# Kernel optimization log

Hardware: AMD Instinct MI355X
Metric: run time of the kernel (lower is better)

Reference implementation:

```python
import jax, jax.numpy as jnp
import numpy as np
import math

B, N, D, SEQ = 4, 1024, 512, 256
HID, DIST_D, N_NER, N_LAB = 150, 128, 3, 4
SPANS_PER_WORD = 0.5
ASPECT, OPINION = 1, 2
NUM_DIST_EMB = 512


def setup_inputs() -> dict:
    key = jax.random.key(0)
    ks = jax.random.split(key, 9)
    starts = jax.random.randint(ks[0], (B, N), 0, SEQ)
    widths = jax.random.randint(ks[1], (B, N), 0, 8)
    ends = jnp.clip(starts + widths, 0, SEQ - 1)
    spans = jnp.stack([starts, ends], axis=-1).astype(jnp.int32)  # [B,N,2]
    ner_scores = jax.random.normal(ks[2], (B, N, N_NER), jnp.float32)
    span_embeddings = jax.random.normal(ks[3], (B, N, D), jnp.float32)
    span_mask = jnp.ones((B, N), dtype=bool)

    pair_dim = 2 * D + DIST_D

    def xavier(k, shape):
        std = math.sqrt(2.0 / (shape[0] + shape[1]))
        return jax.random.normal(k, shape, jnp.float32) * std

    dist_table = xavier(ks[4], (NUM_DIST_EMB, DIST_D))
    W1 = xavier(ks[5], (pair_dim, HID)); b1 = jnp.zeros((HID,), jnp.float32)
    W2 = xavier(ks[6], (HID, HID));      b2 = jnp.zeros((HID,), jnp.float32)
    Wc = xavier(ks[7], (HID, N_LAB));    bc = jnp.zeros((N_LAB,), jnp.float32)

    return dict(spans=spans, ner_scores=ner_scores, span_embeddings=span_embeddings,
                span_mask=span_mask, seq_length=SEQ, dist_table=dist_table,
                W1=W1, b1=b1, W2=W2, b2=b2, Wc=Wc, bc=bc)


def bucket_values(d, num_identity=4, num_total=10):
    # semi-logscale buckets: [0,1,2,3,4,5-7,8-15,16-31,32-63,64+]
    logspace = jnp.floor(jnp.log2(jnp.maximum(d, 1).astype(jnp.float32))).astype(jnp.int32) + (num_identity - 1)
    return jnp.clip(jnp.where(d <= num_identity, d, logspace), 0, num_total - 1)


def _prune(scores, mask, k):
    masked = jnp.where(mask, scores, jnp.float32(-1e20))
    _, idx = jax.lax.top_k(masked, k)  # [B,k]
    return idx


def reference(spans, ner_scores, span_embeddings, span_mask, seq_length,
              dist_table, W1, b1, W2, b2, Wc, bc):
    bsz, n_spans, d = span_embeddings.shape
    k = min(int(math.ceil(seq_length * SPANS_PER_WORD)), n_spans)

    a_idx = _prune(ner_scores[..., ASPECT], span_mask, k)    # [B,k]
    o_idx = _prune(ner_scores[..., OPINION], span_mask, k)
    a_keep = jnp.ones((bsz, k), dtype=bool)  # uniform seq_length -> all kept
    o_keep = a_keep

    gather = lambda t, i: jnp.take_along_axis(t, i[..., None], axis=1)
    a_emb = gather(span_embeddings, a_idx)   # [B,k,D]
    o_emb = gather(span_embeddings, o_idx)   # [B,k,D]
    spans_a = gather(spans, a_idx)           # [B,k,2]
    spans_o = gather(spans, o_idx)           # [B,k,2]

    # pairwise min span distance -> bucket -> embedding
    dis1 = jnp.abs(spans_a[..., 0][:, :, None] - spans_o[..., 1][:, None, :])
    dis2 = jnp.abs(spans_a[..., 1][:, :, None] - spans_o[..., 0][:, None, :])
    dis = jnp.minimum(dis1, dis2)                      # [B,k,k]
    dist_emb = dist_table[bucket_values(dis)]          # [B,k,k,DIST_D]

    pair = jnp.concatenate([
        jnp.broadcast_to(a_emb[:, :, None, :], (bsz, k, k, d)),
        jnp.broadcast_to(o_emb[:, None, :, :], (bsz, k, k, d)),
        dist_emb,
    ], axis=-1)                                        # [B,k,k,2D+DIST_D]

    # FeedForward (2 layers, ReLU, dropout=identity at eval) + classifier
    h = jax.nn.relu(pair @ W1 + b1)
    h = jax.nn.relu(h @ W2 + b2)
    scores = h @ Wc + bc                               # [B,k,k,n_labels]

    rel_mask = a_keep[:, :, None] & o_keep[:, None, :]
    return (jax.nn.softmax(scores, axis=-1), rel_mask, pair, spans_a, spans_o)
```

## Files before the change

### kernel.cpp

```cpp
#include <hip/hip_runtime.h>
#include <hip/hip_bf16.h>

#define BB 4
#define NN 1024
#define DD 512
#define KK 128
#define HID 150
#define HIDP 160
#define HSTRIDE 168
#define DIST_D 128
#define PAIRD 1152

typedef __attribute__((ext_vector_type(4))) float f32x4;
typedef __attribute__((ext_vector_type(8))) short s16x8;

__global__ __launch_bounds__(1024) void k_topk(const int* __restrict__ spans,
                                               const float* __restrict__ ner,
                                               const float* __restrict__ dist_table,
                                               const float* __restrict__ W1,
                                               const float* __restrict__ b1,
                                               const float* __restrict__ W2,
                                               int* ws_aidx, int* ws_oidx,
                                               int* ws_sa, int* ws_so,
                                               float* ws_cd, __hip_bfloat16* ws_w2t,
                                               float* out3, float* out4) {
    int t = threadIdx.x;
    int bx = blockIdx.x;
    if (bx < 8) {
        __shared__ unsigned long long sk[NN];
        int b = bx >> 1;
        int which = bx & 1;
        int ch = which ? 2 : 1;
        float v = ner[(b * NN + t) * 3 + ch];
        unsigned int u = __float_as_uint(v);
        unsigned int s = (u & 0x80000000u) ? ~u : (u ^ 0x80000000u);
        sk[t] = ((unsigned long long)s << 32) | (unsigned int)(NN - 1 - t);
        for (int ksz = 2; ksz <= NN; ksz <<= 1) {
            for (int jsz = ksz >> 1; jsz > 0; jsz >>= 1) {
                __syncthreads();
                int ixj = t ^ jsz;
                if (ixj > t) {
                    unsigned long long k1 = sk[t], k2 = sk[ixj];
                    bool before = k1 > k2;
                    bool desc = ((t & ksz) == 0);
                    if (desc ? !before : before) { sk[t] = k2; sk[ixj] = k1; }
                }
            }
        }
        __syncthreads();
        if (t < KK) {
            int idx = NN - 1 - (int)(unsigned int)(sk[t] & 0xffffffffu);
            int s0 = spans[(b * NN + idx) * 2];
            int s1 = spans[(b * NN + idx) * 2 + 1];
            int row = b * KK + t;
            if (which == 0) {
                ws_aidx[row] = idx;
                ws_sa[row * 2] = s0; ws_sa[row * 2 + 1] = s1;
                out3[row * 2] = (float)s0; out3[row * 2 + 1] = (float)s1;
            } else {
                ws_oidx[row] = idx;
                ws_so[row * 2] = s0; ws_so[row * 2 + 1] = s1;
                out4[row * 2] = (float)s0; out4[row * 2 + 1] = (float)s1;
            }
        }
    } else if (bx < 18) {
        int bk = bx - 8;
        if (t < HIDP) {
            float acc = 0.f;
            if (t < HID) {
                acc = b1[t];
                for (int d = 0; d < DIST_D; ++d)
                    acc = fmaf(dist_table[bk * DIST_D + d], W1[(size_t)(2 * DD + d) * HID + t], acc);
            }
            ws_cd[bk * HIDP + t] = acc;
        }
    } else {
        int e = (bx - 18) * 1024 + t;
        if (e < HIDP * HSTRIDE) {
            int n = e / HSTRIDE, d = e - n * HSTRIDE;
            float v = (n < HID && d < HID) ? W2[d * HID + n] : 0.f;
            ws_w2t[e] = __float2bfloat16(v);
        }
    }
}

__global__ __launch_bounds__(256) void k_contrib(const float* __restrict__ emb,
                                                 const float* __restrict__ W1,
                                                 const int* __restrict__ ws_aidx,
                                                 const int* __restrict__ ws_oidx,
                                                 float* ws_ca, float* ws_co) {
    __shared__ __align__(16) float es[4][DD];
    int t = threadIdx.x;
    int bx = blockIdx.x;
    int which = bx >> 7;
    int row0 = (bx & 127) * 4;
    const int* idxsrc = which ? ws_oidx : ws_aidx;
    for (int x = t; x < 512; x += 256) {
        int r = x >> 7, c = x & 127;
        int row = row0 + r;
        int b = row >> 7;
        int idx = idxsrc[row];
        ((float4*)es[r])[c] = ((const float4*)(emb + ((size_t)(b * NN) + idx) * DD))[c];
    }
    __syncthreads();
    if (t < HIDP) {
        float a0 = 0.f, a1 = 0.f, a2 = 0.f, a3 = 0.f;
        if (t < HID) {
            const float* w = W1 + (size_t)(which * DD) * HID + t;
#pragma unroll 4
            for (int d4 = 0; d4 < 128; ++d4) {
                float4 e0 = ((const float4*)es[0])[d4];
                float4 e1 = ((const float4*)es[1])[d4];
                float4 e2 = ((const float4*)es[2])[d4];
                float4 e3 = ((const float4*)es[3])[d4];
                float w0 = w[(size_t)(4 * d4 + 0) * HID];
                float w1v = w[(size_t)(4 * d4 + 1) * HID];
                float w2v = w[(size_t)(4 * d4 + 2) * HID];
                float w3 = w[(size_t)(4 * d4 + 3) * HID];
                a0 = fmaf(e0.x, w0, a0); a0 = fmaf(e0.y, w1v, a0); a0 = fmaf(e0.z, w2v, a0); a0 = fmaf(e0.w, w3, a0);
                a1 = fmaf(e1.x, w0, a1); a1 = fmaf(e1.y, w1v, a1); a1 = fmaf(e1.z, w2v, a1); a1 = fmaf(e1.w, w3, a1);
                a2 = fmaf(e2.x, w0, a2); a2 = fmaf(e2.y, w1v, a2); a2 = fmaf(e2.z, w2v, a2); a2 = fmaf(e2.w, w3, a2);
                a3 = fmaf(e3.x, w0, a3); a3 = fmaf(e3.y, w1v, a3); a3 = fmaf(e3.z, w2v, a3); a3 = fmaf(e3.w, w3, a3);
            }
        }
        float* dstb = which ? ws_co : ws_ca;
        dstb[(row0 + 0) * HIDP + t] = a0;
        dstb[(row0 + 1) * HIDP + t] = a1;
        dstb[(row0 + 2) * HIDP + t] = a2;
        dstb[(row0 + 3) * HIDP + t] = a3;
    }
}

__global__ __launch_bounds__(256) void k_pair(const float* __restrict__ emb,
                                              const float* __restrict__ dist_table,
                                              const int* __restrict__ ws_aidx,
                                              const int* __restrict__ ws_oidx,
                                              const int* __restrict__ ws_sa,
                                              const int* __restrict__ ws_so,
                                              float* __restrict__ out1,
                                              float* __restrict__ out2) {
    int t = threadIdx.x;
    int blk = blockIdx.x;
    int bi = blk >> 3, jc = blk & 7;
    int b = bi >> 7;
    int j0 = jc << 4;
    int c = t & 127;
    int half = t >> 7;

    const float4* ebase = (const float4*)(emb + (size_t)b * NN * DD);

    int aidx = ws_aidx[bi];
    float4 areg = ebase[(size_t)aidx * 128 + c];

    float4 oreg[8];
#pragma unroll
    for (int it = 0; it < 8; ++it) {
        int j = it * 2 + half;
        int oidx = ws_oidx[b * KK + j0 + j];
        oreg[it] = ebase[(size_t)oidx * 128 + c];
    }

    int sa0 = ws_sa[bi * 2], sa1 = ws_sa[bi * 2 + 1];
    float4 dreg[2];
    int dj[2], dc[2];
#pragma unroll
    for (int it = 0; it < 2; ++it) {
        int x = it * 256 + t;
        dj[it] = x >> 5; dc[it] = x & 31;
        int so0 = ws_so[(b * KK + j0 + dj[it]) * 2];
        int so1 = ws_so[(b * KK + j0 + dj[it]) * 2 + 1];
        int dd = min(abs(sa0 - so1), abs(sa1 - so0));
        int bkt = (dd <= 4) ? dd : min(34 - __clz(dd), 9);
        dreg[it] = ((const float4*)dist_table)[bkt * 32 + dc[it]];
    }

    if (t < 16) out1[bi * KK + j0 + t] = 1.0f;

    float4* dst = (float4*)(out2 + (size_t)bi * (KK * PAIRD)) + (size_t)j0 * 288;
#pragma unroll
    for (int it = 0; it < 8; ++it) {
        int j = it * 2 + half;
        dst[j * 288 + c] = areg;
        dst[j * 288 + 128 + c] = oreg[it];
    }
#pragma unroll
    for (int it = 0; it < 2; ++it) {
        dst[dj[it] * 288 + 256 + dc[it]] = dreg[it];
    }
}

__global__ __launch_bounds__(256) void k_score(const float* __restrict__ Wc,
                                               const float* __restrict__ bcp,
                                               const float* __restrict__ b2p,
                                               const int* __restrict__ ws_sa,
                                               const int* __restrict__ ws_so,
                                               const float* __restrict__ ws_ca,
                                               const float* __restrict__ ws_co,
                                               const float* __restrict__ ws_cd,
                                               const __hip_bfloat16* __restrict__ ws_w2t,
                                               float* __restrict__ out0) {
    __shared__ float ca_s[HIDP];
    __shared__ float wc_s[HID * 4];
    __shared__ float b2_s[HIDP];
    __shared__ float bc_s[4];
    __shared__ int bkt_s[KK];
    __shared__ __align__(16) __hip_bfloat16 h1_s[KK * HSTRIDE];

    int t = threadIdx.x;
    int bi = blockIdx.x;
    int b = bi >> 7;

    if (t < HIDP) ca_s[t] = ws_ca[bi * HIDP + t];
    int sa0 = ws_sa[bi * 2], sa1 = ws_sa[bi * 2 + 1];
    if (t < KK) {
        int so0 = ws_so[(b * KK + t) * 2], so1 = ws_so[(b * KK + t) * 2 + 1];
        int dd = min(abs(sa0 - so1), abs(sa1 - so0));
        bkt_s[t] = (dd <= 4) ? dd : min(34 - __clz(dd), 9);
    }
    for (int x = t; x < HID * 4; x += 256) wc_s[x] = Wc[x];
    if (t < HIDP) b2_s[t] = (t < HID) ? b2p[t] : 0.f;
    if (t < 4) bc_s[t] = bcp[t];
    __syncthreads();

    for (int x = t; x < KK * HIDP; x += 256) {
        int j = x / HIDP, n = x - j * HIDP;
        float v = ca_s[n] + ws_co[(size_t)(b * KK + j) * HIDP + n] + ws_cd[bkt_s[j] * HIDP + n];
        h1_s[j * HSTRIDE + n] = __float2bfloat16(fmaxf(v, 0.f));
    }
    __syncthreads();

    int wave = t >> 6, l = t & 63;
    int lc = l & 15, lg = l >> 4;
    f32x4 acc[2][10];
#pragma unroll
    for (int mi = 0; mi < 2; ++mi)
#pragma unroll
        for (int nt = 0; nt < 10; ++nt)
            acc[mi][nt] = (f32x4){0.f, 0.f, 0.f, 0.f};

#pragma unroll
    for (int kk = 0; kk < 5; ++kk) {
        s16x8 af0 = *(const s16x8*)&h1_s[(wave * 32 + lc) * HSTRIDE + kk * 32 + lg * 8];
        s16x8 af1 = *(const s16x8*)&h1_s[(wave * 32 + 16 + lc) * HSTRIDE + kk * 32 + lg * 8];
#pragma unroll
        for (int nt = 0; nt < 10; ++nt) {
            s16x8 bf = *(const s16x8*)&ws_w2t[(nt * 16 + lc) * HSTRIDE + kk * 32 + lg * 8];
            acc[0][nt] = __builtin_amdgcn_mfma_f32_16x16x32_bf16(af0, bf, acc[0][nt], 0, 0, 0);
            acc[1][nt] = __builtin_amdgcn_mfma_f32_16x16x32_bf16(af1, bf, acc[1][nt], 0, 0, 0);
        }
    }

#pragma unroll
    for (int mi = 0; mi < 2; ++mi) {
#pragma unroll
        for (int r = 0; r < 4; ++r) {
            int j = wave * 32 + mi * 16 + lg * 4 + r;
            float p0 = 0.f, p1 = 0.f, p2 = 0.f, p3 = 0.f;
#pragma unroll
            for (int nt = 0; nt < 10; ++nt) {
                int n = nt * 16 + lc;
                if (n < HID) {
                    float h2 = fmaxf(acc[mi][nt][r] + b2_s[n], 0.f);
                    p0 = fmaf(h2, wc_s[n * 4 + 0], p0);
                    p1 = fmaf(h2, wc_s[n * 4 + 1], p1);
                    p2 = fmaf(h2, wc_s[n * 4 + 2], p2);
                    p3 = fmaf(h2, wc_s[n * 4 + 3], p3);
                }
            }
#pragma unroll
            for (int m = 8; m >= 1; m >>= 1) {
                p0 += __shfl_xor(p0, m, 16);
                p1 += __shfl_xor(p1, m, 16);
                p2 += __shfl_xor(p2, m, 16);
                p3 += __shfl_xor(p3, m, 16);
            }
            p0 += bc_s[0]; p1 += bc_s[1]; p2 += bc_s[2]; p3 += bc_s[3];
            float mx = fmaxf(fmaxf(p0, p1), fmaxf(p2, p3));
            float e0 = expf(p0 - mx), e1 = expf(p1 - mx), e2 = expf(p2 - mx), e3 = expf(p3 - mx);
            float inv = 1.f / (e0 + e1 + e2 + e3);
            if (lc < 4) {
                float v = (lc == 0) ? e0 : (lc == 1) ? e1 : (lc == 2) ? e2 : e3;
                out0[((size_t)bi * KK + j) * 4 + lc] = v * inv;
            }
        }
    }
}

extern "C" void kernel_launch(void* const* d_in, const int* in_sizes, int n_in,
                              void* d_out, int out_size, void* d_ws, size_t ws_size,
                              hipStream_t stream) {
    const int*   spans = (const int*)d_in[0];
    const float* ner   = (const float*)d_in[1];
    const float* emb   = (const float*)d_in[2];
    const float* dist_table = (const float*)d_in[5];
    const float* W1 = (const float*)d_in[6];
    const float* b1 = (const float*)d_in[7];
    const float* W2 = (const float*)d_in[8];
    const float* b2 = (const float*)d_in[9];
    const float* Wc = (const float*)d_in[10];
    const float* bc = (const float*)d_in[11];

    float* out0 = (float*)d_out;
    float* out1 = out0 + (size_t)BB * KK * KK * 4;
    float* out2 = out1 + (size_t)BB * KK * KK;
    float* out3 = out2 + (size_t)BB * KK * KK * PAIRD;
    float* out4 = out3 + (size_t)BB * KK * 2;

    int* ws_aidx = (int*)d_ws;
    int* ws_oidx = ws_aidx + BB * KK;
    int* ws_sa   = ws_oidx + BB * KK;
    int* ws_so   = ws_sa + BB * KK * 2;
    float* ws_ca = (float*)(ws_so + BB * KK * 2);
    float* ws_co = ws_ca + BB * KK * HIDP;
    float* ws_cd = ws_co + BB * KK * HIDP;
    __hip_bfloat16* ws_w2t = (__hip_bfloat16*)(ws_cd + 16 * HIDP);

    k_topk<<<45, 1024, 0, stream>>>(spans, ner, dist_table, W1, b1, W2,
                                    ws_aidx, ws_oidx, ws_sa, ws_so,
                                    ws_cd, ws_w2t, out3, out4);
    k_contrib<<<256, 256, 0, stream>>>(emb, W1, ws_aidx, ws_oidx, ws_ca, ws_co);
    k_pair<<<BB * KK * 8, 256, 0, stream>>>(emb, dist_table, ws_aidx, ws_oidx, ws_sa, ws_so,
                                            out1, out2);
    k_score<<<BB * KK, 256, 0, stream>>>(Wc, bc, b2, ws_sa, ws_so,
                                         ws_ca, ws_co, ws_cd, ws_w2t, out0);
}
```

Measured before the change: 113.4 us.

## Fuse pair-write and score kernels; replace bitonic top-k with rank counting

Merges the pair-tensor writer and the MLP scoring kernel into one launch that interleaves one score block per eight copy blocks, so the compute-bound scoring can overlap the bandwidth-bound pair writes. The first-layer activations are now built directly in MFMA fragment registers from global memory instead of being staged through shared memory, and the weight-transpose row stride changes. Top-k switches from a full bitonic sort with many barriers to each thread counting how many keys exceed its own, giving its rank in a single pass. The cost is more global reads per score wave and O(N) shared-memory reads per thread in top-k.

Result: faster. 104.2 us (-8.1%).

```diff
diff --git a/kernel.cpp b/kernel.cpp
--- a/kernel.cpp
+++ b/kernel.cpp
@@ -7,12 +7,16 @@
 #define KK 128
 #define HID 150
 #define HIDP 160
-#define HSTRIDE 168
+#define W2TS 176
 #define DIST_D 128
 #define PAIRD 1152
 
 typedef __attribute__((ext_vector_type(4))) float f32x4;
 typedef __attribute__((ext_vector_type(8))) short s16x8;
+
+__device__ __forceinline__ int bucket_of(int dd) {
+    return (dd <= 4) ? dd : min(34 - __clz(dd), 9);
+}
 
 __global__ __launch_bounds__(1024) void k_topk(const int* __restrict__ spans,
                                                const float* __restrict__ ner,
@@ -34,25 +38,17 @@
         float v = ner[(b * NN + t) * 3 + ch];
         unsigned int u = __float_as_uint(v);
         unsigned int s = (u & 0x80000000u) ? ~u : (u ^ 0x80000000u);
-        sk[t] = ((unsigned long long)s << 32) | (unsigned int)(NN - 1 - t);
-        for (int ksz = 2; ksz <= NN; ksz <<= 1) {
-            for (int jsz = ksz >> 1; jsz > 0; jsz >>= 1) {
-                __syncthreads();
-                int ixj = t ^ jsz;
-                if (ixj > t) {
-                    unsigned long long k1 = sk[t], k2 = sk[ixj];
-                    bool before = k1 > k2;
-                    bool desc = ((t & ksz) == 0);
-                    if (desc ? !before : before) { sk[t] = k2; sk[ixj] = k1; }
-                }
-            }
-        }
+        unsigned long long mine = ((unsigned long long)s << 32) | (unsigned int)(NN - 1 - t);
+        sk[t] = mine;
         __syncthreads();
-        if (t < KK) {
-            int idx = NN - 1 - (int)(unsigned int)(sk[t] & 0xffffffffu);
+        int cnt = 0;
+#pragma unroll 16
+        for (int d = 0; d < NN; ++d) cnt += (sk[d] > mine) ? 1 : 0;
+        if (cnt < KK) {
+            int idx = t;
             int s0 = spans[(b * NN + idx) * 2];
             int s1 = spans[(b * NN + idx) * 2 + 1];
-            int row = b * KK + t;
+            int row = b * KK + cnt;
             if (which == 0) {
                 ws_aidx[row] = idx;
                 ws_sa[row * 2] = s0; ws_sa[row * 2 + 1] = s1;
@@ -76,8 +72,8 @@
         }
     } else {
         int e = (bx - 18) * 1024 + t;
-        if (e < HIDP * HSTRIDE) {
-            int n = e / HSTRIDE, d = e - n * HSTRIDE;
+        if (e < HIDP * W2TS) {
+            int n = e / W2TS, d = e - n * W2TS;
             float v = (n < HID && d < HID) ? W2[d * HID + n] : 0.f;
             ws_w2t[e] = __float2bfloat16(v);
         }
@@ -131,157 +127,179 @@
     }
 }
 
-__global__ __launch_bounds__(256) void k_pair(const float* __restrict__ emb,
-                                              const float* __restrict__ dist_table,
-                                              const int* __restrict__ ws_aidx,
-                                              const int* __restrict__ ws_oidx,
-                                              const int* __restrict__ ws_sa,
-                                              const int* __restrict__ ws_so,
-                                              float* __restrict__ out1,
-                                              float* __restrict__ out2) {
+__global__ __launch_bounds__(256, 2) void k_fused(const float* __restrict__ emb,
+                                                  const float* __restrict__ dist_table,
+                                                  const float* __restrict__ Wc,
+                                                  const float* __restrict__ bcp,
+                                                  const float* __restrict__ b2p,
+                                                  const int* __restrict__ ws_aidx,
+                                                  const int* __restrict__ ws_oidx,
+                                                  const int* __restrict__ ws_sa,
+                                                  const int* __restrict__ ws_so,
+                                                  const float* __restrict__ ws_ca,
+                                                  const float* __restrict__ ws_co,
+                                                  const float* __restrict__ ws_cd,
+                                                  const __hip_bfloat16* __restrict__ ws_w2t,
+                                                  float* __restrict__ out0,
+                                                  float* __restrict__ out1,
+                                                  float* __restrict__ out2) {
     int t = threadIdx.x;
-    int blk = blockIdx.x;
-    int bi = blk >> 3, jc = blk & 7;
-    int b = bi >> 7;
-    int j0 = jc << 4;
-    int c = t & 127;
-    int half = t >> 7;
-
-    const float4* ebase = (const float4*)(emb + (size_t)b * NN * DD);
-
-    int aidx = ws_aidx[bi];
-    float4 areg = ebase[(size_t)aidx * 128 + c];
-
-    float4 oreg[8];
-#pragma unroll
-    for (int it = 0; it < 8; ++it) {
-        int j = it * 2 + half;
-        int oidx = ws_oidx[b * KK + j0 + j];
-        oreg[it] = ebase[(size_t)oidx * 128 + c];
-    }
-
-    int sa0 = ws_sa[bi * 2], sa1 = ws_sa[bi * 2 + 1];
-    float4 dreg[2];
-    int dj[2], dc[2];
-#pragma unroll
-    for (int it = 0; it < 2; ++it) {
-        int x = it * 256 + t;
-        dj[it] = x >> 5; dc[it] = x & 31;
-        int so0 = ws_so[(b * KK + j0 + dj[it]) * 2];
-        int so1 = ws_so[(b * KK + j0 + dj[it]) * 2 + 1];
-        int dd = min(abs(sa0 - so1), abs(sa1 - so0));
-        int bkt = (dd <= 4) ? dd : min(34 - __clz(dd), 9);
-        dreg[it] = ((const float4*)dist_table)[bkt * 32 + dc[it]];
-    }
-
-    if (t < 16) out1[bi * KK + j0 + t] = 1.0f;
-
-    float4* dst = (float4*)(out2 + (size_t)bi * (KK * PAIRD)) + (size_t)j0 * 288;
-#pragma unroll
-    for (int it = 0; it < 8; ++it) {
-        int j = it * 2 + half;
-        dst[j * 288 + c] = areg;
-        dst[j * 288 + 128 + c] = oreg[it];
-    }
-#pragma unroll
-    for (int it = 0; it < 2; ++it) {
-        dst[dj[it] * 288 + 256 + dc[it]] = dreg[it];
-    }
-}
-
-__global__ __launch_bounds__(256) void k_score(const float* __restrict__ Wc,
-                                               const float* __restrict__ bcp,
-                                               const float* __restrict__ b2p,
-                                               const int* __restrict__ ws_sa,
-                                               const int* __restrict__ ws_so,
-                                               const float* __restrict__ ws_ca,
-                                               const float* __restrict__ ws_co,
-                                               const float* __restrict__ ws_cd,
-                                               const __hip_bfloat16* __restrict__ ws_w2t,
-                                               float* __restrict__ out0) {
-    __shared__ float ca_s[HIDP];
-    __shared__ float wc_s[HID * 4];
-    __shared__ float b2_s[HIDP];
-    __shared__ float bc_s[4];
-    __shared__ int bkt_s[KK];
-    __shared__ __align__(16) __hip_bfloat16 h1_s[KK * HSTRIDE];
-
-    int t = threadIdx.x;
-    int bi = blockIdx.x;
-    int b = bi >> 7;
-
-    if (t < HIDP) ca_s[t] = ws_ca[bi * HIDP + t];
-    int sa0 = ws_sa[bi * 2], sa1 = ws_sa[bi * 2 + 1];
-    if (t < KK) {
-        int so0 = ws_so[(b * KK + t) * 2], so1 = ws_so[(b * KK + t) * 2 + 1];
-        int dd = min(abs(sa0 - so1), abs(sa1 - so0));
-        bkt_s[t] = (dd <= 4) ? dd : min(34 - __clz(dd), 9);
-    }
-    for (int x = t; x < HID * 4; x += 256) wc_s[x] = Wc[x];
-    if (t < HIDP) b2_s[t] = (t < HID) ? b2p[t] : 0.f;
-    if (t < 4) bc_s[t] = bcp[t];
-    __syncthreads();
-
-    for (int x = t; x < KK * HIDP; x += 256) {
-        int j = x / HIDP, n = x - j * HIDP;
-        float v = ca_s[n] + ws_co[(size_t)(b * KK + j) * HIDP + n] + ws_cd[bkt_s[j] * HIDP + n];
-        h1_s[j * HSTRIDE + n] = __float2bfloat16(fmaxf(v, 0.f));
-    }
-    __syncthreads();
-
-    int wave = t >> 6, l = t & 63;
-    int lc = l & 15, lg = l >> 4;
-    f32x4 acc[2][10];
-#pragma unroll
-    for (int mi = 0; mi < 2; ++mi)
-#pragma unroll
-        for (int nt = 0; nt < 10; ++nt)
-            acc[mi][nt] = (f32x4){0.f, 0.f, 0.f, 0.f};
-
-#pragma unroll
-    for (int kk = 0; kk < 5; ++kk) {
-        s16x8 af0 = *(const s16x8*)&h1_s[(wave * 32 + lc) * HSTRIDE + kk * 32 + lg * 8];
-        s16x8 af1 = *(const s16x8*)&h1_s[(wave * 32 + 16 + lc) * HSTRIDE + kk * 32 + lg * 8];
+    int bx = blockIdx.x;
+
+    if (bx >= 4608) {
+        int i = (bx - 4608) * 256 + t;
+        ((float4*)out1)[i] = make_float4(1.f, 1.f, 1.f, 1.f);
+        return;
+    }
+
+    if (bx % 9 == 0) {
+        int bi = bx / 9;
+        int b = bi >> 7;
+        int wave = t >> 6, l = t & 63;
+        int lc = l & 15, lg = l >> 4;
+        int r0 = wave * 32 + lc, r1 = r0 + 16;
+
+        int sa0 = ws_sa[bi * 2], sa1 = ws_sa[bi * 2 + 1];
+        int so00 = ws_so[(b * KK + r0) * 2], so01 = ws_so[(b * KK + r0) * 2 + 1];
+        int so10 = ws_so[(b * KK + r1) * 2], so11 = ws_so[(b * KK + r1) * 2 + 1];
+        int bkt0 = bucket_of(min(abs(sa0 - so01), abs(sa1 - so00)));
+        int bkt1 = bucket_of(min(abs(sa0 - so11), abs(sa1 - so10)));
+
+        const f32x4* ca4 = (const f32x4*)(ws_ca + (size_t)bi * HIDP);
+        const f32x4* co04 = (const f32x4*)(ws_co + (size_t)(b * KK + r0) * HIDP);
+        const f32x4* co14 = (const f32x4*)(ws_co + (size_t)(b * KK + r1) * HIDP);
+        const f32x4* cd04 = (const f32x4*)(ws_cd + (size_t)bkt0 * HIDP);
+        const f32x4* cd14 = (const f32x4*)(ws_cd + (size_t)bkt1 * HIDP);
+
+        s16x8 af0[5], af1[5];
+        union U8 { s16x8 frag; __hip_bfloat16 h[8]; };
+#pragma unroll
+        for (int kk = 0; kk < 5; ++kk) {
+            int o = kk * 8 + lg * 2;
+            f32x4 caa = ca4[o], cab = ca4[o + 1];
+            f32x4 s0a = caa + co04[o] + cd04[o];
+            f32x4 s0b = cab + co04[o + 1] + cd04[o + 1];
+            f32x4 s1a = caa + co14[o] + cd14[o];
+            f32x4 s1b = cab + co14[o + 1] + cd14[o + 1];
+            U8 u0, u1;
+#pragma unroll
+            for (int e = 0; e < 4; ++e) {
+                u0.h[e]     = __float2bfloat16(fmaxf(s0a[e], 0.f));
+                u0.h[e + 4] = __float2bfloat16(fmaxf(s0b[e], 0.f));
+                u1.h[e]     = __float2bfloat16(fmaxf(s1a[e], 0.f));
+                u1.h[e + 4] = __float2bfloat16(fmaxf(s1b[e], 0.f));
+            }
+            af0[kk] = u0.frag;
+            af1[kk] = u1.frag;
+        }
+
+        f32x4 acc[2][10];
+#pragma unroll
+        for (int mi = 0; mi < 2; ++mi)
+#pragma unroll
+            for (int nt = 0; nt < 10; ++nt)
+                acc[mi][nt] = (f32x4){0.f, 0.f, 0.f, 0.f};
+
+#pragma unroll
+        for (int kk = 0; kk < 5; ++kk) {
+#pragma unroll
+            for (int nt = 0; nt < 10; ++nt) {
+                s16x8 bf = *(const s16x8*)&ws_w2t[(nt * 16 + lc) * W2TS + kk * 32 + lg * 8];
+                acc[0][nt] = __builtin_amdgcn_mfma_f32_16x16x32_bf16(af0[kk], bf, acc[0][nt], 0, 0, 0);
+                acc[1][nt] = __builtin_amdgcn_mfma_f32_16x16x32_bf16(af1[kk], bf, acc[1][nt], 0, 0, 0);
+            }
+        }
+
+        float4 wcv[10];
+        float b2v[10];
 #pragma unroll
         for (int nt = 0; nt < 10; ++nt) {
-            s16x8 bf = *(const s16x8*)&ws_w2t[(nt * 16 + lc) * HSTRIDE + kk * 32 + lg * 8];
-            acc[0][nt] = __builtin_amdgcn_mfma_f32_16x16x32_bf16(af0, bf, acc[0][nt], 0, 0, 0);
-            acc[1][nt] = __builtin_amdgcn_mfma_f32_16x16x32_bf16(af1, bf, acc[1][nt], 0, 0, 0);
-        }
-    }
-
-#pragma unroll
-    for (int mi = 0; mi < 2; ++mi) {
-#pragma unroll
-        for (int r = 0; r < 4; ++r) {
-            int j = wave * 32 + mi * 16 + lg * 4 + r;
-            float p0 = 0.f, p1 = 0.f, p2 = 0.f, p3 = 0.f;
-#pragma unroll
-            for (int nt = 0; nt < 10; ++nt) {
-                int n = nt * 16 + lc;
-                if (n < HID) {
-                    float h2 = fmaxf(acc[mi][nt][r] + b2_s[n], 0.f);
-                    p0 = fmaf(h2, wc_s[n * 4 + 0], p0);
-                    p1 = fmaf(h2, wc_s[n * 4 + 1], p1);
-                    p2 = fmaf(h2, wc_s[n * 4 + 2], p2);
-                    p3 = fmaf(h2, wc_s[n * 4 + 3], p3);
+            int n = nt * 16 + lc;
+            if (n < HID) {
+                wcv[nt] = *(const float4*)(Wc + n * 4);
+                b2v[nt] = b2p[n];
+            } else {
+                wcv[nt] = make_float4(0.f, 0.f, 0.f, 0.f);
+                b2v[nt] = 0.f;
+            }
+        }
+        float bc0 = bcp[0], bc1 = bcp[1], bc2 = bcp[2], bc3 = bcp[3];
+
+#pragma unroll
+        for (int mi = 0; mi < 2; ++mi) {
+#pragma unroll
+            for (int r = 0; r < 4; ++r) {
+                int j = wave * 32 + mi * 16 + lg * 4 + r;
+                float p0 = 0.f, p1 = 0.f, p2 = 0.f, p3 = 0.f;
+#pragma unroll
+                for (int nt = 0; nt < 10; ++nt) {
+                    float h2 = fmaxf(acc[mi][nt][r] + b2v[nt], 0.f);
+                    p0 = fmaf(h2, wcv[nt].x, p0);
+                    p1 = fmaf(h2, wcv[nt].y, p1);
+                    p2 = fmaf(h2, wcv[nt].z, p2);
+                    p3 = fmaf(h2, wcv[nt].w, p3);
                 }
-            }
-#pragma unroll
-            for (int m = 8; m >= 1; m >>= 1) {
-                p0 += __shfl_xor(p0, m, 16);
-                p1 += __shfl_xor(p1, m, 16);
-                p2 += __shfl_xor(p2, m, 16);
-                p3 += __shfl_xor(p3, m, 16);
-            }
-            p0 += bc_s[0]; p1 += bc_s[1]; p2 += bc_s[2]; p3 += bc_s[3];
-            float mx = fmaxf(fmaxf(p0, p1), fmaxf(p2, p3));
-            float e0 = expf(p0 - mx), e1 = expf(p1 - mx), e2 = expf(p2 - mx), e3 = expf(p3 - mx);
-            float inv = 1.f / (e0 + e1 + e2 + e3);
-            if (lc < 4) {
-                float v = (lc == 0) ? e0 : (lc == 1) ? e1 : (lc == 2) ? e2 : e3;
-                out0[((size_t)bi * KK + j) * 4 + lc] = v * inv;
-            }
+#pragma unroll
+                for (int m = 8; m >= 1; m >>= 1) {
+                    p0 += __shfl_xor(p0, m, 16);
+                    p1 += __shfl_xor(p1, m, 16);
+                    p2 += __shfl_xor(p2, m, 16);
+                    p3 += __shfl_xor(p3, m, 16);
+                }
+                p0 += bc0; p1 += bc1; p2 += bc2; p3 += bc3;
+                float mx = fmaxf(fmaxf(p0, p1), fmaxf(p2, p3));
+                float e0 = expf(p0 - mx), e1 = expf(p1 - mx), e2 = expf(p2 - mx), e3 = expf(p3 - mx);
+                float inv = 1.f / (e0 + e1 + e2 + e3);
+                if (lc < 4) {
+                    float v = (lc == 0) ? e0 : (lc == 1) ? e1 : (lc == 2) ? e2 : e3;
+                    out0[((size_t)bi * KK + j) * 4 + lc] = v * inv;
+                }
+            }
+        }
+    } else {
+        int pid = bx - bx / 9 - 1;
+        int bi = pid >> 3, jc = pid & 7;
+        int b = bi >> 7;
+        int j0 = jc << 4;
+        int c = t & 127;
+        int half = t >> 7;
+
+        const float4* ebase = (const float4*)(emb + (size_t)b * NN * DD);
+
+        int aidx = ws_aidx[bi];
+        float4 areg = ebase[(size_t)aidx * 128 + c];
+
+        float4 oreg[8];
+#pragma unroll
+        for (int it = 0; it < 8; ++it) {
+            int j = it * 2 + half;
+            int oidx = ws_oidx[b * KK + j0 + j];
+            oreg[it] = ebase[(size_t)oidx * 128 + c];
+        }
+
+        int sa0 = ws_sa[bi * 2], sa1 = ws_sa[bi * 2 + 1];
+        float4 dreg[2];
+        int dj[2], dc[2];
+#pragma unroll
+        for (int it = 0; it < 2; ++it) {
+            int x = it * 256 + t;
+            dj[it] = x >> 5; dc[it] = x & 31;
+            int so0 = ws_so[(b * KK + j0 + dj[it]) * 2];
+            int so1 = ws_so[(b * KK + j0 + dj[it]) * 2 + 1];
+            int bkt = bucket_of(min(abs(sa0 - so1), abs(sa1 - so0)));
+            dreg[it] = ((const float4*)dist_table)[bkt * 32 + dc[it]];
+        }
+
+        float4* dst = (float4*)(out2 + (size_t)bi * (KK * PAIRD)) + (size_t)j0 * 288;
+#pragma unroll
+        for (int it = 0; it < 8; ++it) {
+            int j = it * 2 + half;
+            dst[j * 288 + c] = areg;
+            dst[j * 288 + 128 + c] = oreg[it];
+        }
+#pragma unroll
+        for (int it = 0; it < 2; ++it) {
+            dst[dj[it] * 288 + 256 + dc[it]] = dreg[it];
         }
     }
 }
@@ -315,12 +333,12 @@
     float* ws_cd = ws_co + BB * KK * HIDP;
     __hip_bfloat16* ws_w2t = (__hip_bfloat16*)(ws_cd + 16 * HIDP);
 
-    k_topk<<<45, 1024, 0, stream>>>(spans, ner, dist_table, W1, b1, W2,
+    k_topk<<<46, 1024, 0, stream>>>(spans, ner, dist_table, W1, b1, W2,
                                     ws_aidx, ws_oidx, ws_sa, ws_so,
                                     ws_cd, ws_w2t, out3, out4);
     k_contrib<<<256, 256, 0, stream>>>(emb, W1, ws_aidx, ws_oidx, ws_ca, ws_co);
-    k_pair<<<BB * KK * 8, 256, 0, stream>>>(emb, dist_table, ws_aidx, ws_oidx, ws_sa, ws_so,
-                                            out1, out2);
-    k_score<<<BB * KK, 256, 0, stream>>>(Wc, bc, b2, ws_sa, ws_so,
-                                         ws_ca, ws_co, ws_cd, ws_w2t, out0);
-}
+    k_fused<<<4672, 256, 0, stream>>>(emb, dist_table, Wc, bc, b2,
+                                      ws_aidx, ws_oidx, ws_sa, ws_so,
+                                      ws_ca, ws_co, ws_cd, ws_w2t,
+                                      out0, out1, out2);
+}
```
